# Kernel tuning notes

Measured on AMD Instinct MI355X. Metric: run time of the kernel, lower is better.

The kernel has to match this reference:

```python
import jax, jax.numpy as jnp
import numpy as np

N_NODES = 50000
N_EDGES = 300000
HEADS = 2
OUT_CH = 128
BN_EPS = 1e-5
NEG_SLOPE = 0.2


def _batchnorm(x, g, b):
    # training-mode BatchNorm1d: biased batch statistics
    mean = x.mean(axis=0)
    var = x.var(axis=0)
    return (x - mean) * jax.lax.rsqrt(var + BN_EPS) * g + b


def _gatv2(x, src, dst, edge_attr, Wl, bl, Wr, br, We, att, bias, concat):
    # PyG GATv2Conv, share_weights=False, aggr='add'
    n = x.shape[0]
    xl = (x @ Wl + bl).reshape(n, HEADS, OUT_CH)  # source messages
    xr = (x @ Wr + br).reshape(n, HEADS, OUT_CH)  # destination term
    ee = (edge_attr @ We).reshape(-1, HEADS, OUT_CH)
    s = jax.nn.leaky_relu(xl[src] + xr[dst] + ee, NEG_SLOPE)  # [E,H,C]
    alpha = jnp.einsum('ehc,hc->eh', s, att)  # [E,H]
    # segment softmax over edges grouped by destination node
    m = jax.ops.segment_max(alpha, dst, num_segments=n)
    a = jnp.exp(alpha - m[dst])
    den = jax.ops.segment_sum(a, dst, num_segments=n)
    a = a / (den[dst] + 1e-16)
    out = jax.ops.segment_sum(xl[src] * a[:, :, None], dst, num_segments=n)  # [N,H,C]
    out = out.reshape(n, HEADS * OUT_CH) if concat else out.mean(axis=1)
    return out + bias


def setup_inputs() -> dict:
    key = jax.random.key(0)
    ks = jax.random.split(key, 16)
    d = {}
    d['h'] = jax.random.normal(ks[0], (N_NODES, 5), jnp.float32)
    d['edge_index'] = jax.random.randint(ks[1], (2, N_EDGES), 0, N_NODES, jnp.int64)
    d['edge_weight'] = jax.random.uniform(ks[2], (N_EDGES, 1), jnp.float32)
    d['bn0_g'] = jnp.ones((5,), jnp.float32)
    d['bn0_b'] = jnp.zeros((5,), jnp.float32)
    d['bn1_g'] = jnp.ones((256,), jnp.float32)
    d['bn1_b'] = jnp.zeros((256,), jnp.float32)
    def lin(k, fan_in, fan_out):
        return jax.random.normal(k, (fan_in, fan_out), jnp.float32) * (1.0 / np.sqrt(fan_in))
    # conv1: in=5 -> heads*out=256, concat=True
    d['c1_Wl'] = lin(ks[3], 5, 256); d['c1_bl'] = jnp.zeros((256,), jnp.float32)
    d['c1_Wr'] = lin(ks[4], 5, 256); d['c1_br'] = jnp.zeros((256,), jnp.float32)
    d['c1_We'] = lin(ks[5], 1, 256)
    d['c1_att'] = jax.random.normal(ks[6], (HEADS, OUT_CH), jnp.float32) * 0.1
    d['c1_bias'] = jnp.zeros((256,), jnp.float32)
    # mu: in=256 -> 128, concat=False
    d['mu_Wl'] = lin(ks[7], 256, 256); d['mu_bl'] = jnp.zeros((256,), jnp.float32)
    d['mu_Wr'] = lin(ks[8], 256, 256); d['mu_br'] = jnp.zeros((256,), jnp.float32)
    d['mu_We'] = lin(ks[9], 1, 256)
    d['mu_att'] = jax.random.normal(ks[10], (HEADS, OUT_CH), jnp.float32) * 0.1
    d['mu_bias'] = jnp.zeros((128,), jnp.float32)
    # log_std: same shapes as mu
    d['ls_Wl'] = lin(ks[11], 256, 256); d['ls_bl'] = jnp.zeros((256,), jnp.float32)
    d['ls_Wr'] = lin(ks[12], 256, 256); d['ls_br'] = jnp.zeros((256,), jnp.float32)
    d['ls_We'] = lin(ks[13], 1, 256)
    d['ls_att'] = jax.random.normal(ks[14], (HEADS, OUT_CH), jnp.float32) * 0.1
    d['ls_bias'] = jnp.zeros((128,), jnp.float32)
    return d


def reference(h, edge_index, edge_weight, bn0_g, bn0_b, bn1_g, bn1_b,
              c1_Wl, c1_bl, c1_Wr, c1_br, c1_We, c1_att, c1_bias,
              mu_Wl, mu_bl, mu_Wr, mu_br, mu_We, mu_att, mu_bias,
              ls_Wl, ls_bl, ls_Wr, ls_br, ls_We, ls_att, ls_bias):
    src, dst = edge_index[0], edge_index[1]
    x = _batchnorm(h, bn0_g, bn0_b)
    x = _gatv2(x, src, dst, edge_weight, c1_Wl, c1_bl, c1_Wr, c1_br, c1_We, c1_att, c1_bias, concat=True)
    x = jax.nn.relu(_batchnorm(x, bn1_g, bn1_b))
    # dropout identity (eval / deterministic)
    mu = _gatv2(x, src, dst, edge_weight, mu_Wl, mu_bl, mu_Wr, mu_br, mu_We, mu_att, mu_bias, concat=False)
    log_std = _gatv2(x, src, dst, edge_weight, ls_Wl, ls_bl, ls_Wr, ls_br, ls_We, ls_att, ls_bias, concat=False)
    return (mu, log_std)
```

## Files before the change

### kernel.cpp

```cpp
#include <hip/hip_runtime.h>
#include <math.h>

#define N_NODES 50000
#define N_EDGES 300000
#define BN_EPS 1e-5f
#define NEG_SLOPE 0.2f

#define RB_COUNT 3128
#define SCAN_TILES 49
#define BN1_BLOCKS 523
#define K5_BLOCKS 1024

#define AGG_BLOCKS 2048
#define AGG_STRIDE (AGG_BLOCKS * 4)

#define PREP_BN0 128
#define PREP_EC  1172
#define PREP_PW  128

typedef short bf8v __attribute__((ext_vector_type(8)));
typedef float f4v __attribute__((ext_vector_type(4)));
typedef float f2v __attribute__((ext_vector_type(2)));

__device__ inline unsigned short f2bf(float f) {
    union { float f; unsigned u; } c; c.f = f;
    unsigned r = c.u + 0x7fffu + ((c.u >> 16) & 1u);
    return (unsigned short)(r >> 16);
}

__device__ inline unsigned f2bf2(float lo, float hi) {
    return (unsigned)f2bf(lo) | ((unsigned)f2bf(hi) << 16);
}

__device__ inline f2v bfpair(unsigned u) {
    union { unsigned u; float f; } lo, hi;
    lo.u = u << 16;
    hi.u = u & 0xffff0000u;
    f2v r; r.x = lo.f; r.y = hi.f;
    return r;
}

__device__ inline void async_copy16(void* lds, const void* g) {
    __builtin_amdgcn_global_load_lds(
        (const __attribute__((address_space(1))) unsigned int*)g,
        (__attribute__((address_space(3))) unsigned int*)lds, 16, 0, 0);
}

__global__ __launch_bounds__(256) void prep(
        const float* __restrict__ h, float* __restrict__ acc,
        const int* __restrict__ dst, int* __restrict__ count,
        const float* __restrict__ Wl0, const float* __restrict__ Wr0,
        const float* __restrict__ Wl1, const float* __restrict__ Wr1,
        unsigned short* __restrict__ bp) {
    int b = blockIdx.x;
    if (b < PREP_BN0) {
        __shared__ float lds[4][10];
        int tid = threadIdx.x;
        int lane = tid & 63, wave = tid >> 6;
        float ls[5] = {0,0,0,0,0}, lq[5] = {0,0,0,0,0};
        for (int r = b * 256 + tid; r < N_NODES; r += PREP_BN0 * 256) {
            #pragma unroll
            for (int k = 0; k < 5; k++) {
                float v = h[r*5 + k];
                ls[k] += v; lq[k] += v*v;
            }
        }
        #pragma unroll
        for (int k = 0; k < 5; k++) {
            #pragma unroll
            for (int m = 1; m <= 32; m <<= 1) {
                ls[k] += __shfl_xor(ls[k], m, 64);
                lq[k] += __shfl_xor(lq[k], m, 64);
            }
        }
        if (lane == 0) {
            #pragma unroll
            for (int k = 0; k < 5; k++) { lds[wave][k] = ls[k]; lds[wave][5+k] = lq[k]; }
        }
        __syncthreads();
        if (tid < 10) {
            float s = lds[0][tid] + lds[1][tid] + lds[2][tid] + lds[3][tid];
            atomicAdd(&acc[tid], s);
        }
    } else if (b < PREP_BN0 + PREP_EC) {
        int e = (b - PREP_BN0) * 256 + threadIdx.x;
        if (e < N_EDGES) atomicAdd(&count[dst[e]], 1);
    } else {
        int t = (b - PREP_BN0 - PREP_EC) * 256 + threadIdx.x;
        int lane = t & 63;
        int nt = (t >> 6) & 31;
        int kc = (t >> 11) & 7;
        int conv = t >> 14;
        int col = nt * 16 + (lane & 15);
        int k0 = kc * 32 + (lane >> 4) * 8;
        const float* W = conv ? (col < 256 ? Wl1 : Wr1) : (col < 256 ? Wl0 : Wr0);
        int c = col & 255;
        union { unsigned short h[8]; uint4 u; } tmp;
        #pragma unroll
        for (int j = 0; j < 8; j++) tmp.h[j] = f2bf(W[(size_t)(k0 + j) * 256 + c]);
        *reinterpret_cast<uint4*>(bp + (size_t)t * 8) = tmp.u;
    }
}

__global__ void local_scan(const int* __restrict__ count, int* __restrict__ offsets,
                           int* __restrict__ tileSum) {
    __shared__ int wsum[16];
    int tid = threadIdx.x;
    int lane = tid & 63, wv = tid >> 6;
    int i = blockIdx.x * 1024 + tid;
    int v = (i < N_NODES) ? count[i] : 0;
    int inc = v;
    #pragma unroll
    for (int off = 1; off < 64; off <<= 1) {
        int t = __shfl_up(inc, off, 64);
        if (lane >= off) inc += t;
    }
    if (lane == 63) wsum[wv] = inc;
    __syncthreads();
    if (wv == 0) {
        int val = (lane < 16) ? wsum[lane] : 0;
        int inc2 = val;
        #pragma unroll
        for (int off = 1; off < 16; off <<= 1) {
            int t = __shfl_up(inc2, off, 64);
            if (lane >= off) inc2 += t;
        }
        if (lane < 16) wsum[lane] = inc2 - val;
    }
    __syncthreads();
    int excl = inc - v + wsum[wv];
    if (i < N_NODES) offsets[i] = excl;
    if (tid == 1023) tileSum[blockIdx.x] = excl + v;
}

__global__ void add_prefix(int* __restrict__ offsets, const int* __restrict__ tileSum,
                           int* __restrict__ cursor) {
    __shared__ int spref;
    int tid = threadIdx.x;
    if (tid < 64) {
        int v = (tid < blockIdx.x) ? tileSum[tid] : 0;
        #pragma unroll
        for (int m = 1; m <= 32; m <<= 1) v += __shfl_xor(v, m, 64);
        if (tid == 0) spref = v;
    }
    __syncthreads();
    int i = blockIdx.x * 1024 + tid;
    if (i < N_NODES) {
        int o = offsets[i] + spref;
        offsets[i] = o;
        cursor[i] = o;
    }
    if (blockIdx.x == 0 && tid == 0) offsets[N_NODES] = N_EDGES;
}

__global__ void edge_scatter(const int* __restrict__ dst, const int* __restrict__ src,
                             const float* __restrict__ ew, int* __restrict__ cursor,
                             int2* __restrict__ sep) {
    int e = blockIdx.x * blockDim.x + threadIdx.x;
    if (e < N_EDGES) {
        int pos = atomicAdd(&cursor[dst[e]], 1);
        sep[pos] = make_int2(src[e], __float_as_int(ew[e]));
    }
}

__global__ __launch_bounds__(128) void gemm_k5(const float* __restrict__ h,
        const float* __restrict__ acc10, const float* __restrict__ g5,
        const float* __restrict__ b5,
        const float* __restrict__ Wl, const float* __restrict__ bl,
        const float* __restrict__ Wr, const float* __restrict__ br,
        unsigned short* __restrict__ xl, unsigned short* __restrict__ xr) {
    int c = threadIdx.x * 2;
    float sc[5], sh[5];
    #pragma unroll
    for (int k = 0; k < 5; k++) {
        float mean = acc10[k] * (1.f / N_NODES);
        float var  = acc10[5 + k] * (1.f / N_NODES) - mean * mean;
        float s = g5[k] * rsqrtf(var + BN_EPS);
        sc[k] = s; sh[k] = b5[k] - mean * s;
    }
    float wl0[5], wl1[5], wr0[5], wr1[5];
    #pragma unroll
    for (int k = 0; k < 5; k++) {
        wl0[k] = Wl[k*256 + c]; wl1[k] = Wl[k*256 + c + 1];
        wr0[k] = Wr[k*256 + c]; wr1[k] = Wr[k*256 + c + 1];
    }
    float bl0 = bl[c], bl1 = bl[c+1], br0 = br[c], br1 = br[c+1];
    int n = blockIdx.x;
    float hv[5];
    if (n < N_NODES) {
        #pragma unroll
        for (int k = 0; k < 5; k++) hv[k] = h[n*5 + k];
    }
    for (; n < N_NODES; n += K5_BLOCKS) {
        int n2 = n + K5_BLOCKS;
        float hn[5] = {0,0,0,0,0};
        if (n2 < N_NODES) {
            #pragma unroll
            for (int k = 0; k < 5; k++) hn[k] = h[n2*5 + k];
        }
        float l0 = bl0, l1 = bl1, r0 = br0, r1 = br1;
        #pragma unroll
        for (int k = 0; k < 5; k++) {
            float a = hv[k] * sc[k] + sh[k];
            l0 += a * wl0[k]; l1 += a * wl1[k];
            r0 += a * wr0[k]; r1 += a * wr1[k];
        }
        *reinterpret_cast<unsigned*>(xl + (size_t)n*256 + c) = f2bf2(l0, l1);
        *reinterpret_cast<unsigned*>(xr + (size_t)n*256 + c) = f2bf2(r0, r1);
        #pragma unroll
        for (int k = 0; k < 5; k++) hv[k] = hn[k];
    }
}

__global__ __launch_bounds__(512, 4) void gemm_mfma(const unsigned short* __restrict__ xh,
        const float* __restrict__ ss1,
        const unsigned short* __restrict__ bp,
        const float* __restrict__ bl0, const float* __restrict__ br0,
        const float* __restrict__ bl1, const float* __restrict__ br1,
        unsigned short* __restrict__ xlA, unsigned short* __restrict__ xrA,
        unsigned short* __restrict__ xlB, unsigned short* __restrict__ xrB) {
    __shared__ unsigned short Bs[2][32][512];
    int cv = blockIdx.x >= 782;
    int bb = cv ? blockIdx.x - 782 : blockIdx.x;
    int lane = threadIdx.x & 63;
    int wave = threadIdx.x >> 6;
    int h = wave & 1;
    int rb = bb * 4 + (wave >> 1);

    const unsigned short* bsrc = bp + (size_t)cv * 131072 + lane * 8;
    auto stage = [&](int buf, int kc) {
        #pragma unroll
        for (int j = 0; j < 4; j++) {
            int f = wave * 4 + j;
            async_copy16(&Bs[buf][f][lane * 8], bsrc + (size_t)kc * 16384 + f * 512);
        }
    };
    stage(0, 0);

    int row = rb * 16 + (lane & 15);
    int k0b = (lane >> 4) * 8;
    bool rok = row < N_NODES;
    bf8v a[8];
    #pragma unroll
    for (int kc = 0; kc < 8; kc++) {
        int k0 = kc * 32 + k0b;
        union { unsigned short hh[8]; uint4 u; bf8v v; } tmp;
        if (rok) {
            uint4 u = *(const uint4*)(xh + (size_t)row * 256 + k0);
            f4v s0 = *(const f4v*)(ss1 + k0);
            f4v s1 = *(const f4v*)(ss1 + k0 + 4);
            f4v h0 = *(const f4v*)(ss1 + 256 + k0);
            f4v h1 = *(const f4v*)(ss1 + 256 + k0 + 4);
            float f[8];
            f2v p;
            p = bfpair(u.x); f[0] = p.x; f[1] = p.y;
            p = bfpair(u.y); f[2] = p.x; f[3] = p.y;
            p = bfpair(u.z); f[4] = p.x; f[5] = p.y;
            p = bfpair(u.w); f[6] = p.x; f[7] = p.y;
            float scv[8] = {s0.x, s0.y, s0.z, s0.w, s1.x, s1.y, s1.z, s1.w};
            float shv[8] = {h0.x, h0.y, h0.z, h0.w, h1.x, h1.y, h1.z, h1.w};
            #pragma unroll
            for (int j = 0; j < 8; j++) {
                float v = f[j] * scv[j] + shv[j];
                v = v > 0.f ? v : 0.f;
                tmp.hh[j] = f2bf(v);
            }
        } else {
            tmp.u = (uint4){0u, 0u, 0u, 0u};
        }
        a[kc] = tmp.v;
    }

    f4v acc[16];
    #pragma unroll
    for (int t = 0; t < 16; t++) acc[t] = (f4v){0.f, 0.f, 0.f, 0.f};

    for (int kc = 0; kc < 8; kc++) {
        __syncthreads();
        if (kc < 7) stage((kc + 1) & 1, kc + 1);
        const unsigned short* bb2 = &Bs[kc & 1][h * 16][lane * 8];
        #pragma unroll
        for (int t = 0; t < 16; t++) {
            bf8v b = *reinterpret_cast<const bf8v*>(bb2 + t * 512);
            acc[t] = __builtin_amdgcn_mfma_f32_16x16x32_bf16(b, a[kc], acc[t], 0, 0, 0);
        }
    }

    int q = lane >> 4;
    unsigned short* outp = cv ? (h ? xrB : xlB) : (h ? xrA : xlA);
    const float* bias = cv ? (h ? br1 : bl1) : (h ? br0 : bl0);
    if (rok) {
        unsigned short* orow = outp + (size_t)row * 256 + q * 4;
        #pragma unroll
        for (int t = 0; t < 16; t++) {
            f4v bv = *(const f4v*)(bias + t * 16 + q * 4);
            uint2 u;
            u.x = f2bf2(acc[t][0] + bv.x, acc[t][1] + bv.y);
            u.y = f2bf2(acc[t][2] + bv.z, acc[t][3] + bv.w);
            *reinterpret_cast<uint2*>(orow + t * 16) = u;
        }
    }
}

__global__ __launch_bounds__(256) void agg_concat(
        const unsigned short* __restrict__ xl, const unsigned short* __restrict__ xr,
        const float* __restrict__ We, const float* __restrict__ att,
        const int* __restrict__ offsets, const int2* __restrict__ sep,
        const float* __restrict__ bias,
        unsigned short* __restrict__ outh) {
    int gw = blockIdx.x * 4 + (threadIdx.x >> 6);
    int lane = threadIdx.x & 63;
    int half = lane >> 5;
    int sub  = lane & 31;
    int cb   = (sub >> 4) * 128 + (sub & 15) * 8;
    f2v wv[4], av[4];
    float bs[8];
    {
        f4v t0 = *(const f4v*)(We + cb);
        f4v t1 = *(const f4v*)(We + cb + 4);
        wv[0] = (f2v){t0.x, t0.y}; wv[1] = (f2v){t0.z, t0.w};
        wv[2] = (f2v){t1.x, t1.y}; wv[3] = (f2v){t1.z, t1.w};
        t0 = *(const f4v*)(att + cb);
        t1 = *(const f4v*)(att + cb + 4);
        av[0] = (f2v){t0.x, t0.y}; av[1] = (f2v){t0.z, t0.w};
        av[2] = (f2v){t1.x, t1.y}; av[3] = (f2v){t1.z, t1.w};
        t0 = *(const f4v*)(bias + cb);
        t1 = *(const f4v*)(bias + cb + 4);
        bs[0]=t0.x; bs[1]=t0.y; bs[2]=t0.z; bs[3]=t0.w;
        bs[4]=t1.x; bs[5]=t1.y; bs[6]=t1.z; bs[7]=t1.w;
    }
    int n = gw;
    int beg = 0, end = 0;
    if (n < N_NODES) { beg = offsets[n]; end = offsets[n + 1]; }
    while (n < N_NODES) {
        int nn = n + AGG_STRIDE;
        int nbeg = 0, nend = 0;
        if (nn < N_NODES) { nbeg = offsets[nn]; nend = offsets[nn + 1]; }
        uint4 r8 = *(const uint4*)(xr + ((size_t)n << 8) + cb);
        f2v rv[4];
        rv[0] = bfpair(r8.x); rv[1] = bfpair(r8.y);
        rv[2] = bfpair(r8.z); rv[3] = bfpair(r8.w);

        float den = 0.f;
        f2v acc[4];
        #pragma unroll
        for (int j = 0; j < 4; j++) acc[j] = (f2v){0.f, 0.f};

        int i = beg + half;
        float wN = 0.f;
        int2 seP = make_int2(0, 0);
        uint4 lN = {0u, 0u, 0u, 0u};
        if (i < end) {
            int2 se = sep[i];
            wN = __int_as_float(se.y);
            lN = *(const uint4*)(xl + ((size_t)se.x << 8) + cb);
        }
        if (i + 2 < end) seP = sep[i + 2];
        for (; i < end; i += 2) {
            uint4 l8 = lN; float w = wN;
            if (i + 2 < end) {
                lN = *(const uint4*)(xl + ((size_t)seP.x << 8) + cb);
                wN = __int_as_float(seP.y);
            }
            if (i + 4 < end) seP = sep[i + 4];
            f2v w2 = (f2v){w, w};
            f2v lv[4];
            lv[0] = bfpair(l8.x); lv[1] = bfpair(l8.y);
            lv[2] = bfpair(l8.z); lv[3] = bfpair(l8.w);
            f2v da = (f2v){0.f, 0.f};
            #pragma unroll
            for (int j = 0; j < 4; j++) {
                f2v v = lv[j] + rv[j] + w2 * wv[j];
                f2v s = v * (f2v){NEG_SLOPE, NEG_SLOPE};
                v.x = fmaxf(v.x, s.x); v.y = fmaxf(v.y, s.y);
                da += v * av[j];
            }
            float a = da.x + da.y;
            a += __shfl_xor(a, 1, 64);
            a += __shfl_xor(a, 2, 64);
            a += __shfl_xor(a, 4, 64);
            a += __shfl_xor(a, 8, 64);
            float p = __expf(a);
            den += p;
            f2v p2 = (f2v){p, p};
            #pragma unroll
            for (int j = 0; j < 4; j++) acc[j] += p2 * lv[j];
        }
        den += __shfl_xor(den, 32, 64);
        #pragma unroll
        for (int j = 0; j < 4; j++) {
            f2v ao;
            ao.x = __shfl_xor(acc[j].x, 32, 64);
            ao.y = __shfl_xor(acc[j].y, 32, 64);
            acc[j] += ao;
        }
        float inv = 1.f / (den + 1e-16f);
        if (lane < 32) {
            union { unsigned short hh[8]; uint4 u; } o;
            #pragma unroll
            for (int j = 0; j < 4; j++) {
                o.hh[2*j]   = f2bf(acc[j].x * inv + bs[2*j]);
                o.hh[2*j+1] = f2bf(acc[j].y * inv + bs[2*j + 1]);
            }
            *(uint4*)(outh + (size_t)n * 256 + cb) = o.u;
        }
        n = nn; beg = nbeg; end = nend;
    }
}

__global__ __launch_bounds__(256) void agg_dual(
        const unsigned short* __restrict__ xlA, const unsigned short* __restrict__ xrA,
        const unsigned short* __restrict__ xlB, const unsigned short* __restrict__ xrB,
        const float* __restrict__ WeA, const float* __restrict__ attA,
        const float* __restrict__ WeB, const float* __restrict__ attB,
        const int* __restrict__ offsets, const int2* __restrict__ sep,
        const float* __restrict__ biasA, const float* __restrict__ biasB,
        float* __restrict__ outA, float* __restrict__ outB) {
    int gw = blockIdx.x * 4 + (threadIdx.x >> 6);
    int lane = threadIdx.x & 63;
    int half = lane >> 5;
    int sub  = lane & 31;
    int cb   = (sub >> 4) * 128 + (sub & 15) * 8;
    int c0 = (lane & 15) * 8;
    f2v wvA[4], avA[4], wvB[4], avB[4];
    float bsv[8];
    {
        f4v t0 = *(const f4v*)(WeA + cb);
        f4v t1 = *(const f4v*)(WeA + cb + 4);
        wvA[0] = (f2v){t0.x, t0.y}; wvA[1] = (f2v){t0.z, t0.w};
        wvA[2] = (f2v){t1.x, t1.y}; wvA[3] = (f2v){t1.z, t1.w};
        t0 = *(const f4v*)(attA + cb);
        t1 = *(const f4v*)(attA + cb + 4);
        avA[0] = (f2v){t0.x, t0.y}; avA[1] = (f2v){t0.z, t0.w};
        avA[2] = (f2v){t1.x, t1.y}; avA[3] = (f2v){t1.z, t1.w};
        t0 = *(const f4v*)(WeB + cb);
        t1 = *(const f4v*)(WeB + cb + 4);
        wvB[0] = (f2v){t0.x, t0.y}; wvB[1] = (f2v){t0.z, t0.w};
        wvB[2] = (f2v){t1.x, t1.y}; wvB[3] = (f2v){t1.z, t1.w};
        t0 = *(const f4v*)(attB + cb);
        t1 = *(const f4v*)(attB + cb + 4);
        avB[0] = (f2v){t0.x, t0.y}; avB[1] = (f2v){t0.z, t0.w};
        avB[2] = (f2v){t1.x, t1.y}; avB[3] = (f2v){t1.z, t1.w};
        const float* bp = (lane < 32) ? biasA : biasB;
        f4v b0 = *(const f4v*)(bp + c0);
        f4v b1 = *(const f4v*)(bp + c0 + 4);
        bsv[0]=b0.x; bsv[1]=b0.y; bsv[2]=b0.z; bsv[3]=b0.w;
        bsv[4]=b1.x; bsv[5]=b1.y; bsv[6]=b1.z; bsv[7]=b1.w;
    }
    int n = gw;
    int beg = 0, end = 0;
    if (n < N_NODES) { beg = offsets[n]; end = offsets[n + 1]; }
    while (n < N_NODES) {
        int nn = n + AGG_STRIDE;
        int nbeg = 0, nend = 0;
        if (nn < N_NODES) { nbeg = offsets[nn]; nend = offsets[nn + 1]; }
        uint4 r8A = *(const uint4*)(xrA + ((size_t)n << 8) + cb);
        uint4 r8B = *(const uint4*)(xrB + ((size_t)n << 8) + cb);
        f2v rvA[4], rvB[4];
        rvA[0] = bfpair(r8A.x); rvA[1] = bfpair(r8A.y);
        rvA[2] = bfpair(r8A.z); rvA[3] = bfpair(r8A.w);
        rvB[0] = bfpair(r8B.x); rvB[1] = bfpair(r8B.y);
        rvB[2] = bfpair(r8B.z); rvB[3] = bfpair(r8B.w);

        float dA = 0.f, dB = 0.f;
        f2v accA[4], accB[4];
        #pragma unroll
        for (int j = 0; j < 4; j++) { accA[j] = (f2v){0.f, 0.f}; accB[j] = (f2v){0.f, 0.f}; }

        int i = beg + half;
        float wN = 0.f;
        int2 seP = make_int2(0, 0);
        uint4 lNA = {0u, 0u, 0u, 0u}, lNB = {0u, 0u, 0u, 0u};
        if (i < end) {
            int2 se = sep[i];
            wN = __int_as_float(se.y);
            size_t o = ((size_t)se.x << 8) + cb;
            lNA = *(const uint4*)(xlA + o);
            lNB = *(const uint4*)(xlB + o);
        }
        if (i + 2 < end) seP = sep[i + 2];
        for (; i < end; i += 2) {
            uint4 lA = lNA, lB = lNB; float w = wN;
            if (i + 2 < end) {
                size_t o = ((size_t)seP.x << 8) + cb;
                lNA = *(const uint4*)(xlA + o);
                lNB = *(const uint4*)(xlB + o);
                wN = __int_as_float(seP.y);
            }
            if (i + 4 < end) seP = sep[i + 4];
            f2v w2 = (f2v){w, w};
            f2v lvA[4], lvB[4];
            lvA[0] = bfpair(lA.x); lvA[1] = bfpair(lA.y);
            lvA[2] = bfpair(lA.z); lvA[3] = bfpair(lA.w);
            lvB[0] = bfpair(lB.x); lvB[1] = bfpair(lB.y);
            lvB[2] = bfpair(lB.z); lvB[3] = bfpair(lB.w);
            f2v daA = (f2v){0.f, 0.f}, daB = (f2v){0.f, 0.f};
            #pragma unroll
            for (int j = 0; j < 4; j++) {
                f2v vA = lvA[j] + rvA[j] + w2 * wvA[j];
                f2v sA = vA * (f2v){NEG_SLOPE, NEG_SLOPE};
                vA.x = fmaxf(vA.x, sA.x); vA.y = fmaxf(vA.y, sA.y);
                daA += vA * avA[j];
                f2v vB = lvB[j] + rvB[j] + w2 * wvB[j];
                f2v sB = vB * (f2v){NEG_SLOPE, NEG_SLOPE};
                vB.x = fmaxf(vB.x, sB.x); vB.y = fmaxf(vB.y, sB.y);
                daB += vB * avB[j];
            }
            float aA = daA.x + daA.y, aB = daB.x + daB.y;
            float tA, tB;
            tA = __shfl_xor(aA, 1, 64); tB = __shfl_xor(aB, 1, 64); aA += tA; aB += tB;
            tA = __shfl_xor(aA, 2, 64); tB = __shfl_xor(aB, 2, 64); aA += tA; aB += tB;
            tA = __shfl_xor(aA, 4, 64); tB = __shfl_xor(aB, 4, 64); aA += tA; aB += tB;
            tA = __shfl_xor(aA, 8, 64); tB = __shfl_xor(aB, 8, 64); aA += tA; aB += tB;
            float pA = __expf(aA), pB = __expf(aB);
            dA += pA; dB += pB;
            f2v pA2 = (f2v){pA, pA}, pB2 = (f2v){pB, pB};
            #pragma unroll
            for (int j = 0; j < 4; j++) {
                accA[j] += pA2 * lvA[j];
                accB[j] += pB2 * lvB[j];
            }
        }
        dA += __shfl_xor(dA, 32, 64);
        dB += __shfl_xor(dB, 32, 64);
        #pragma unroll
        for (int j = 0; j < 4; j++) {
            f2v ao;
            ao.x = __shfl_xor(accA[j].x, 32, 64);
            ao.y = __shfl_xor(accA[j].y, 32, 64);
            accA[j] += ao;
            ao.x = __shfl_xor(accB[j].x, 32, 64);
            ao.y = __shfl_xor(accB[j].y, 32, 64);
            accB[j] += ao;
        }
        float invA = 1.f / (dA + 1e-16f);
        float invB = 1.f / (dB + 1e-16f);
        float oA[8], oB[8], poA[8], poB[8];
        #pragma unroll
        for (int j = 0; j < 4; j++) {
            oA[2*j]   = accA[j].x * invA;
            oA[2*j+1] = accA[j].y * invA;
            oB[2*j]   = accB[j].x * invB;
            oB[2*j+1] = accB[j].y * invB;
        }
        #pragma unroll
        for (int j = 0; j < 8; j++) {
            poA[j] = __shfl_xor(oA[j], 16, 64);
            poB[j] = __shfl_xor(oB[j], 16, 64);
        }
        int q = lane >> 4;
        if (q == 0) {
            float r[8];
            #pragma unroll
            for (int j = 0; j < 8; j++) r[j] = (oA[j] + poA[j]) * 0.5f + bsv[j];
            *(float4*)(outA + (size_t)n * 128 + c0)     = *(float4*)&r[0];
            *(float4*)(outA + (size_t)n * 128 + c0 + 4) = *(float4*)&r[4];
        } else if (q == 2) {
            float r[8];
            #pragma unroll
            for (int j = 0; j < 8; j++) r[j] = (oB[j] + poB[j]) * 0.5f + bsv[j];
            *(float4*)(outB + (size_t)n * 128 + c0)     = *(float4*)&r[0];
            *(float4*)(outB + (size_t)n * 128 + c0 + 4) = *(float4*)&r[4];
        }
        n = nn; beg = nbeg; end = nend;
    }
}

__global__ void bn1_reduce(const unsigned short* __restrict__ xh, float* __restrict__ part) {
    __shared__ float lds[256][9];
    int tid = threadIdx.x;
    int cg = tid & 63;
    int ph = tid >> 6;
    int r0 = blockIdx.x * 96;
    float s[4] = {0,0,0,0}, q[4] = {0,0,0,0};
    #pragma unroll
    for (int it = 0; it < 24; it++) {
        int row = r0 + it * 4 + ph;
        if (row < N_NODES) {
            uint2 v = *(const uint2*)(xh + (size_t)row * 256 + cg * 4);
            f2v p0 = bfpair(v.x), p1 = bfpair(v.y);
            s[0] += p0.x; s[1] += p0.y; s[2] += p1.x; s[3] += p1.y;
            q[0] += p0.x*p0.x; q[1] += p0.y*p0.y; q[2] += p1.x*p1.x; q[3] += p1.y*p1.y;
        }
    }
    #pragma unroll
    for (int j = 0; j < 4; j++) { lds[tid][j] = s[j]; lds[tid][4+j] = q[j]; }
    __syncthreads();
    if (tid < 64) {
        float4 sv, qv;
        float* svp = (float*)&sv; float* qvp = (float*)&qv;
        #pragma unroll
        for (int j = 0; j < 4; j++) {
            svp[j] = lds[tid][j] + lds[tid+64][j] + lds[tid+128][j] + lds[tid+192][j];
            qvp[j] = lds[tid][4+j] + lds[tid+64][4+j] + lds[tid+128][4+j] + lds[tid+192][4+j];
        }
        *(float4*)(part + (size_t)blockIdx.x * 512 + cg * 4) = sv;
        *(float4*)(part + (size_t)blockIdx.x * 512 + 256 + cg * 4) = qv;
    }
}

__global__ void bn1_finalize(const float* __restrict__ part, const float* __restrict__ g,
                             const float* __restrict__ b, float* __restrict__ ss1) {
    __shared__ float lds[8][64];
    int t = threadIdx.x;
    int c = blockIdx.x * 32 + (t & 31);
    int ph = t >> 5;
    float s = 0.f, q = 0.f;
    for (int bi = ph; bi < BN1_BLOCKS; bi += 8) {
        s += part[(size_t)bi * 512 + c];
        q += part[(size_t)bi * 512 + 256 + c];
    }
    lds[ph][t & 31] = s;
    lds[ph][32 + (t & 31)] = q;
    __syncthreads();
    if (t < 32) {
        float ss = 0.f, qq = 0.f;
        #pragma unroll
        for (int p = 0; p < 8; p++) { ss += lds[p][t]; qq += lds[p][32 + t]; }
        float mean = ss * (1.f / N_NODES);
        float var  = qq * (1.f / N_NODES) - mean * mean;
        float sc = g[c] * rsqrtf(var + BN_EPS);
        ss1[c] = sc;
        ss1[256 + c] = b[c] - mean * sc;
    }
}

extern "C" void kernel_launch(void* const* d_in, const int* in_sizes, int n_in,
                              void* d_out, int out_size, void* d_ws, size_t ws_size,
                              hipStream_t stream) {
    const float* h          = (const float*)d_in[0];
    const int*   edge_index = (const int*)d_in[1];
    const int*   src = edge_index;
    const int*   dst = edge_index + N_EDGES;
    const float* ew   = (const float*)d_in[2];
    const float* bn0g = (const float*)d_in[3];
    const float* bn0b = (const float*)d_in[4];
    const float* bn1g = (const float*)d_in[5];
    const float* bn1b = (const float*)d_in[6];
    const float* c1_Wl = (const float*)d_in[7];
    const float* c1_bl = (const float*)d_in[8];
    const float* c1_Wr = (const float*)d_in[9];
    const float* c1_br = (const float*)d_in[10];
    const float* c1_We = (const float*)d_in[11];
    const float* c1_att = (const float*)d_in[12];
    const float* c1_bias = (const float*)d_in[13];
    const float* mu_Wl = (const float*)d_in[14];
    const float* mu_bl = (const float*)d_in[15];
    const float* mu_Wr = (const float*)d_in[16];
    const float* mu_br = (const float*)d_in[17];
    const float* mu_We = (const float*)d_in[18];
    const float* mu_att = (const float*)d_in[19];
    const float* mu_bias = (const float*)d_in[20];
    const float* ls_Wl = (const float*)d_in[21];
    const float* ls_bl = (const float*)d_in[22];
    const float* ls_Wr = (const float*)d_in[23];
    const float* ls_br = (const float*)d_in[24];
    const float* ls_We = (const float*)d_in[25];
    const float* ls_att = (const float*)d_in[26];
    const float* ls_bias = (const float*)d_in[27];

    float* out_mu = (float*)d_out;
    float* out_ls = (float*)d_out + (size_t)N_NODES * 128;

    char* ws = (char*)d_ws;
    size_t off = 0;
    auto alloc = [&](size_t bytes) -> void* {
        void* p = ws + off;
        off += (bytes + 255) / 256 * 256;
        return p;
    };
    unsigned short* xl  = (unsigned short*)alloc((size_t)N_NODES * 256 * 2);
    unsigned short* xr  = (unsigned short*)alloc((size_t)N_NODES * 256 * 2);
    unsigned short* xBh = (unsigned short*)alloc((size_t)N_NODES * 256 * 2);
    unsigned short* xl2 = (unsigned short*)alloc((size_t)N_NODES * 256 * 2);
    unsigned short* xr2 = (unsigned short*)alloc((size_t)N_NODES * 256 * 2);
    float* bn0acc  = (float*)alloc(10 * 4);
    float* bn1part = (float*)alloc((size_t)BN1_BLOCKS * 512 * 4);
    float* bn1ss   = (float*)alloc(512 * 4);
    int*   count   = (int*)alloc((size_t)N_NODES * 4);
    int*   offsets = (int*)alloc((size_t)(N_NODES + 1) * 4);
    int*   cursor  = (int*)alloc((size_t)N_NODES * 4);
    int2*  sep     = (int2*)alloc((size_t)N_EDGES * 8);
    int*   tileSum = (int*)alloc((size_t)SCAN_TILES * 4);
    unsigned short* Bpack = (unsigned short*)alloc((size_t)2 * 131072 * 2);

    hipMemsetAsync(count, 0, (size_t)N_NODES * 4, stream);
    hipMemsetAsync(bn0acc, 0, 10 * 4, stream);

    prep<<<PREP_BN0 + PREP_EC + PREP_PW, 256, 0, stream>>>(
        h, bn0acc, dst, count, mu_Wl, mu_Wr, ls_Wl, ls_Wr, Bpack);

    local_scan<<<SCAN_TILES, 1024, 0, stream>>>(count, offsets, tileSum);
    add_prefix<<<SCAN_TILES, 1024, 0, stream>>>(offsets, tileSum, cursor);
    edge_scatter<<<(N_EDGES + 255) / 256, 256, 0, stream>>>(dst, src, ew, cursor, sep);

    gemm_k5<<<K5_BLOCKS, 128, 0, stream>>>(h, bn0acc, bn0g, bn0b,
                                           c1_Wl, c1_bl, c1_Wr, c1_br, xl, xr);
    agg_concat<<<AGG_BLOCKS, 256, 0, stream>>>(xl, xr, c1_We, c1_att, offsets,
                                               sep, c1_bias, xBh);

    bn1_reduce<<<BN1_BLOCKS, 256, 0, stream>>>(xBh, bn1part);
    bn1_finalize<<<8, 256, 0, stream>>>(bn1part, bn1g, bn1b, bn1ss);

    gemm_mfma<<<1564, 512, 0, stream>>>(xBh, bn1ss, Bpack,
                                        mu_bl, mu_br, ls_bl, ls_br,
                                        xl, xr, xl2, xr2);

    agg_dual<<<AGG_BLOCKS, 256, 0, stream>>>(xl, xr, xl2, xr2,
                                             mu_We, mu_att, ls_We, ls_att,
                                             offsets, sep,
                                             mu_bias, ls_bias, out_mu, out_ls);
}
```

Before: 416.7 us.

## Split agg_dual wavefront halves by conv instead of by edge parity

The dual aggregation kernel now assigns the lower 32 lanes to conv A and the upper 32 to conv B. Each half walks every edge of the node sequentially, instead of both halves processing both convs on alternating edges. This roughly halves the per-lane register state and removes the cross-half reduction of accumulators. Launch bounds are raised to request 8 blocks per SM for higher occupancy. In exchange, each half-wave loops over twice as many edges, which lengthens the serial dependency chain per node.

```diff
diff --git a/kernel.cpp b/kernel.cpp
--- a/kernel.cpp
+++ b/kernel.cpp
@@ -408,7 +408,7 @@
     }
 }
 
-__global__ __launch_bounds__(256) void agg_dual(
+__global__ __launch_bounds__(256, 8) void agg_dual(
         const unsigned short* __restrict__ xlA, const unsigned short* __restrict__ xrA,
         const unsigned short* __restrict__ xlB, const unsigned short* __restrict__ xrB,
         const float* __restrict__ WeA, const float* __restrict__ attA,
@@ -418,34 +418,24 @@
         float* __restrict__ outA, float* __restrict__ outB) {
     int gw = blockIdx.x * 4 + (threadIdx.x >> 6);
     int lane = threadIdx.x & 63;
-    int half = lane >> 5;
     int sub  = lane & 31;
     int cb   = (sub >> 4) * 128 + (sub & 15) * 8;
-    int c0 = (lane & 15) * 8;
-    f2v wvA[4], avA[4], wvB[4], avB[4];
-    float bsv[8];
+    int c0   = (lane & 15) * 8;
+    int convB = lane >> 5;
+    const unsigned short* xlp = (convB ? xlB : xlA) + cb;
+    const unsigned short* xrp = (convB ? xrB : xrA) + cb;
+    const float* Wep  = convB ? WeB : WeA;
+    const float* attp = convB ? attB : attA;
+    f2v wv[4], av[4];
     {
-        f4v t0 = *(const f4v*)(WeA + cb);
-        f4v t1 = *(const f4v*)(WeA + cb + 4);
-        wvA[0] = (f2v){t0.x, t0.y}; wvA[1] = (f2v){t0.z, t0.w};
-        wvA[2] = (f2v){t1.x, t1.y}; wvA[3] = (f2v){t1.z, t1.w};
-        t0 = *(const f4v*)(attA + cb);
-        t1 = *(const f4v*)(attA + cb + 4);
-        avA[0] = (f2v){t0.x, t0.y}; avA[1] = (f2v){t0.z, t0.w};
-        avA[2] = (f2v){t1.x, t1.y}; avA[3] = (f2v){t1.z, t1.w};
-        t0 = *(const f4v*)(WeB + cb);
-        t1 = *(const f4v*)(WeB + cb + 4);
-        wvB[0] = (f2v){t0.x, t0.y}; wvB[1] = (f2v){t0.z, t0.w};
-        wvB[2] = (f2v){t1.x, t1.y}; wvB[3] = (f2v){t1.z, t1.w};
-        t0 = *(const f4v*)(attB + cb);
-        t1 = *(const f4v*)(attB + cb + 4);
-        avB[0] = (f2v){t0.x, t0.y}; avB[1] = (f2v){t0.z, t0.w};
-        avB[2] = (f2v){t1.x, t1.y}; avB[3] = (f2v){t1.z, t1.w};
-        const float* bp = (lane < 32) ? biasA : biasB;
-        f4v b0 = *(const f4v*)(bp + c0);
-        f4v b1 = *(const f4v*)(bp + c0 + 4);
-        bsv[0]=b0.x; bsv[1]=b0.y; bsv[2]=b0.z; bsv[3]=b0.w;
-        bsv[4]=b1.x; bsv[5]=b1.y; bsv[6]=b1.z; bsv[7]=b1.w;
+        f4v t0 = *(const f4v*)(Wep + cb);
+        f4v t1 = *(const f4v*)(Wep + cb + 4);
+        wv[0] = (f2v){t0.x, t0.y}; wv[1] = (f2v){t0.z, t0.w};
+        wv[2] = (f2v){t1.x, t1.y}; wv[3] = (f2v){t1.z, t1.w};
+        t0 = *(const f4v*)(attp + cb);
+        t1 = *(const f4v*)(attp + cb + 4);
+        av[0] = (f2v){t0.x, t0.y}; av[1] = (f2v){t0.z, t0.w};
+        av[2] = (f2v){t1.x, t1.y}; av[3] = (f2v){t1.z, t1.w};
     }
     int n = gw;
     int beg = 0, end = 0;
@@ -454,111 +444,84 @@
         int nn = n + AGG_STRIDE;
         int nbeg = 0, nend = 0;
         if (nn < N_NODES) { nbeg = offsets[nn]; nend = offsets[nn + 1]; }
-        uint4 r8A = *(const uint4*)(xrA + ((size_t)n << 8) + cb);
-        uint4 r8B = *(const uint4*)(xrB + ((size_t)n << 8) + cb);
-        f2v rvA[4], rvB[4];
-        rvA[0] = bfpair(r8A.x); rvA[1] = bfpair(r8A.y);
-        rvA[2] = bfpair(r8A.z); rvA[3] = bfpair(r8A.w);
-        rvB[0] = bfpair(r8B.x); rvB[1] = bfpair(r8B.y);
-        rvB[2] = bfpair(r8B.z); rvB[3] = bfpair(r8B.w);
-
-        float dA = 0.f, dB = 0.f;
-        f2v accA[4], accB[4];
-        #pragma unroll
-        for (int j = 0; j < 4; j++) { accA[j] = (f2v){0.f, 0.f}; accB[j] = (f2v){0.f, 0.f}; }
-
-        int i = beg + half;
-        float wN = 0.f;
-        int2 seP = make_int2(0, 0);
-        uint4 lNA = {0u, 0u, 0u, 0u}, lNB = {0u, 0u, 0u, 0u};
+        uint4 r8 = *(const uint4*)(xrp + ((size_t)n << 8));
+        f2v rv[4];
+        rv[0] = bfpair(r8.x); rv[1] = bfpair(r8.y);
+        rv[2] = bfpair(r8.z); rv[3] = bfpair(r8.w);
+
+        float den = 0.f;
+        f2v acc[4];
+        #pragma unroll
+        for (int j = 0; j < 4; j++) acc[j] = (f2v){0.f, 0.f};
+
+        int i = beg;
+        float wN = 0.f, wP = 0.f;
+        int sP = 0;
+        uint4 lN = {0u, 0u, 0u, 0u};
         if (i < end) {
             int2 se = sep[i];
             wN = __int_as_float(se.y);
-            size_t o = ((size_t)se.x << 8) + cb;
-            lNA = *(const uint4*)(xlA + o);
-            lNB = *(const uint4*)(xlB + o);
-        }
-        if (i + 2 < end) seP = sep[i + 2];
-        for (; i < end; i += 2) {
-            uint4 lA = lNA, lB = lNB; float w = wN;
-            if (i + 2 < end) {
-                size_t o = ((size_t)seP.x << 8) + cb;
-                lNA = *(const uint4*)(xlA + o);
-                lNB = *(const uint4*)(xlB + o);
-                wN = __int_as_float(seP.y);
-            }
-            if (i + 4 < end) seP = sep[i + 4];
+            lN = *(const uint4*)(xlp + ((size_t)se.x << 8));
+        }
+        if (i + 1 < end) { int2 se = sep[i + 1]; sP = se.x; wP = __int_as_float(se.y); }
+        for (; i < end; ++i) {
+            uint4 l8 = lN; float w = wN;
+            if (i + 1 < end) {
+                lN = *(const uint4*)(xlp + ((size_t)sP << 8));
+                wN = wP;
+            }
+            if (i + 2 < end) { int2 se = sep[i + 2]; sP = se.x; wP = __int_as_float(se.y); }
             f2v w2 = (f2v){w, w};
-            f2v lvA[4], lvB[4];
-            lvA[0] = bfpair(lA.x); lvA[1] = bfpair(lA.y);
-            lvA[2] = bfpair(lA.z); lvA[3] = bfpair(lA.w);
-            lvB[0] = bfpair(lB.x); lvB[1] = bfpair(lB.y);
-            lvB[2] = bfpair(lB.z); lvB[3] = bfpair(lB.w);
-            f2v daA = (f2v){0.f, 0.f}, daB = (f2v){0.f, 0.f};
+            f2v lv[4];
+            lv[0] = bfpair(l8.x); lv[1] = bfpair(l8.y);
+            lv[2] = bfpair(l8.z); lv[3] = bfpair(l8.w);
+            f2v da = (f2v){0.f, 0.f};
             #pragma unroll
             for (int j = 0; j < 4; j++) {
-                f2v vA = lvA[j] + rvA[j] + w2 * wvA[j];
-                f2v sA = vA * (f2v){NEG_SLOPE, NEG_SLOPE};
-                vA.x = fmaxf(vA.x, sA.x); vA.y = fmaxf(vA.y, sA.y);
-                daA += vA * avA[j];
-                f2v vB = lvB[j] + rvB[j] + w2 * wvB[j];
-                f2v sB = vB * (f2v){NEG_SLOPE, NEG_SLOPE};
-                vB.x = fmaxf(vB.x, sB.x); vB.y = fmaxf(vB.y, sB.y);
-                daB += vB * avB[j];
-            }
-            float aA = daA.x + daA.y, aB = daB.x + daB.y;
-            float tA, tB;
-            tA = __shfl_xor(aA, 1, 64); tB = __shfl_xor(aB, 1, 64); aA += tA; aB += tB;
-            tA = __shfl_xor(aA, 2, 64); tB = __shfl_xor(aB, 2, 64); aA += tA; aB += tB;
-            tA = __shfl_xor(aA, 4, 64); tB = __shfl_xor(aB, 4, 64); aA += tA; aB += tB;
-            tA = __shfl_xor(aA, 8, 64); tB = __shfl_xor(aB, 8, 64); aA += tA; aB += tB;
-            float pA = __expf(aA), pB = __expf(aB);
-            dA += pA; dB += pB;
-            f2v pA2 = (f2v){pA, pA}, pB2 = (f2v){pB, pB};
-            #pragma unroll
-            for (int j = 0; j < 4; j++) {
-                accA[j] += pA2 * lvA[j];
-                accB[j] += pB2 * lvB[j];
-            }
-        }
-        dA += __shfl_xor(dA, 32, 64);
-        dB += __shfl_xor(dB, 32, 64);
+                f2v v = lv[j] + rv[j] + w2 * wv[j];
+                f2v s = v * (f2v){NEG_SLOPE, NEG_SLOPE};
+                v.x = fmaxf(v.x, s.x); v.y = fmaxf(v.y, s.y);
+                da += v * av[j];
+            }
+            float a = da.x + da.y;
+            a += __shfl_xor(a, 1, 64);
+            a += __shfl_xor(a, 2, 64);
+            a += __shfl_xor(a, 4, 64);
+            a += __shfl_xor(a, 8, 64);
+            float p = __expf(a);
+            den += p;
+            f2v p2 = (f2v){p, p};
+            #pragma unroll
+            for (int j = 0; j < 4; j++) acc[j] += p2 * lv[j];
+        }
+        float inv = 1.f / (den + 1e-16f);
+        float o[8], po[8];
         #pragma unroll
         for (int j = 0; j < 4; j++) {
-            f2v ao;
-            ao.x = __shfl_xor(accA[j].x, 32, 64);
-            ao.y = __shfl_xor(accA[j].y, 32, 64);
-            accA[j] += ao;
-            ao.x = __shfl_xor(accB[j].x, 32, 64);
-            ao.y = __shfl_xor(accB[j].y, 32, 64);
-            accB[j] += ao;
-        }
-        float invA = 1.f / (dA + 1e-16f);
-        float invB = 1.f / (dB + 1e-16f);
-        float oA[8], oB[8], poA[8], poB[8];
-        #pragma unroll
-        for (int j = 0; j < 4; j++) {
-            oA[2*j]   = accA[j].x * invA;
-            oA[2*j+1] = accA[j].y * invA;
-            oB[2*j]   = accB[j].x * invB;
-            oB[2*j+1] = accB[j].y * invB;
-        }
-        #pragma unroll
-        for (int j = 0; j < 8; j++) {
-            poA[j] = __shfl_xor(oA[j], 16, 64);
-            poB[j] = __shfl_xor(oB[j], 16, 64);
-        }
+            o[2*j]   = acc[j].x * inv;
+            o[2*j+1] = acc[j].y * inv;
+        }
+        #pragma unroll
+        for (int j = 0; j < 8; j++) po[j] = __shfl_xor(o[j], 16, 64);
         int q = lane >> 4;
         if (q == 0) {
+            f4v b0 = *(const f4v*)(biasA + c0);
+            f4v b1 = *(const f4v*)(biasA + c0 + 4);
             float r[8];
-            #pragma unroll
-            for (int j = 0; j < 8; j++) r[j] = (oA[j] + poA[j]) * 0.5f + bsv[j];
+            r[0] = (o[0]+po[0])*0.5f + b0.x; r[1] = (o[1]+po[1])*0.5f + b0.y;
+            r[2] = (o[2]+po[2])*0.5f + b0.z; r[3] = (o[3]+po[3])*0.5f + b0.w;
+            r[4] = (o[4]+po[4])*0.5f + b1.x; r[5] = (o[5]+po[5])*0.5f + b1.y;
+            r[6] = (o[6]+po[6])*0.5f + b1.z; r[7] = (o[7]+po[7])*0.5f + b1.w;
             *(float4*)(outA + (size_t)n * 128 + c0)     = *(float4*)&r[0];
             *(float4*)(outA + (size_t)n * 128 + c0 + 4) = *(float4*)&r[4];
         } else if (q == 2) {
+            f4v b0 = *(const f4v*)(biasB + c0);
+            f4v b1 = *(const f4v*)(biasB + c0 + 4);
             float r[8];
-            #pragma unroll
-            for (int j = 0; j < 8; j++) r[j] = (oB[j] + poB[j]) * 0.5f + bsv[j];
+            r[0] = (o[0]+po[0])*0.5f + b0.x; r[1] = (o[1]+po[1])*0.5f + b0.y;
+            r[2] = (o[2]+po[2])*0.5f + b0.z; r[3] = (o[3]+po[3])*0.5f + b0.w;
+            r[4] = (o[4]+po[4])*0.5f + b1.x; r[5] = (o[5]+po[5])*0.5f + b1.y;
+            r[6] = (o[6]+po[6])*0.5f + b1.z; r[7] = (o[7]+po[7])*0.5f + b1.w;
             *(float4*)(outB + (size_t)n * 128 + c0)     = *(float4*)&r[0];
             *(float4*)(outB + (size_t)n * 128 + c0 + 4) = *(float4*)&r[4];
         }
```

Result: slower. 446.9 us (+7.2%).
